# Kernel optimization log

Measured on AMD Instinct MI355X. Metric: run time of the kernel, lower is better.

## Reference

```python
import jax, jax.numpy as jnp
import numpy as np

NUM_HEADS = 8
KERNEL_SEARCH = 5  # local attention window
EPS = 1e-5


def _layernorm(x, g, b):
    m = jnp.mean(x, axis=-1, keepdims=True)
    v = jnp.var(x, axis=-1, keepdims=True)
    return (x - m) / jnp.sqrt(v + EPS) * g + b


def _unfold3(x):
    # x: [N, C, H, W] -> [N, C*9, H*W]; matches torch F.unfold(kernel=3, pad=1)
    # ordering: channel-major, kernel position (row-major) minor.
    N, C, H, W = x.shape
    xp = jnp.pad(x, ((0, 0), (0, 0), (1, 1), (1, 1)))
    pats = jnp.stack([xp[:, :, i:i + H, j:j + W] for i in range(3) for j in range(3)], axis=2)
    return pats.reshape(N, C * 9, H * W)


def _sai2token(x, w_mlp):
    # x: [b, c, a, h, w] -> tokens [h*w, b*a, spa_dim]
    b, c, a, h, w = x.shape
    x = x.transpose(0, 2, 1, 3, 4).reshape(b * a, c, h, w)
    tok = _unfold3(x).transpose(2, 0, 1)  # [hw, b*a, c*9]
    return jnp.einsum('lnk,ek->lne', tok, w_mlp)


def _local_mask(h, w, k):
    # additive mask [h*w, h*w]: 0 inside local kxk window, -inf outside
    kl, kr = k // 2, k - k // 2
    ii = jnp.arange(h)
    jj = jnp.arange(w)
    okh = (ii[None, :] >= ii[:, None] - kl) & (ii[None, :] < ii[:, None] + kr)  # [h,h]
    okw = (jj[None, :] >= jj[:, None] - kl) & (jj[None, :] < jj[:, None] + kr)  # [w,w]
    ok = okh[:, None, :, None] & okw[None, :, None, :]  # [h,w,h,w]
    ok = ok.reshape(h * w, h * w)
    return jnp.where(ok, 0.0, -jnp.inf).astype(jnp.float32)


def _attention(qk_in, v_in, in_proj_w, out_proj_w, bias):
    # qk_in/v_in: [L, B, E]; torch nn.MultiheadAttention, no biases, eval mode
    L, B, E = qk_in.shape
    Dh = E // NUM_HEADS
    Wq, Wk, Wv = in_proj_w[:E], in_proj_w[E:2 * E], in_proj_w[2 * E:]
    q = jnp.einsum('lbe,fe->lbf', qk_in, Wq).reshape(L, B, NUM_HEADS, Dh)
    k = jnp.einsum('lbe,fe->lbf', qk_in, Wk).reshape(L, B, NUM_HEADS, Dh)
    v = jnp.einsum('lbe,fe->lbf', v_in, Wv).reshape(L, B, NUM_HEADS, Dh)
    scale = 1.0 / np.sqrt(Dh).astype(np.float32)
    scores = jnp.einsum('lbhd,mbhd->bhlm', q, k) * scale + bias[None, None]
    attn = jax.nn.softmax(scores, axis=-1)
    out = jnp.einsum('bhlm,mbhd->lbhd', attn, v).reshape(L, B, E)
    return jnp.einsum('lbe,fe->lbf', out, out_proj_w)


def reference(buffer, spa_position, w_mlp, ln1_g, ln1_b, in_proj_w, out_proj_w,
              ln2_g, ln2_b, ff_w1, ff_w2, conv_w):
    b, c, a, h, w = buffer.shape
    bias = _local_mask(h, w, KERNEL_SEARCH)
    tok = _sai2token(buffer, w_mlp)          # [hw, b*a, E]
    pe = _sai2token(spa_position, w_mlp)
    x = _layernorm(tok + pe, ln1_g, ln1_b)
    tok = _attention(x, tok, in_proj_w, out_proj_w, bias) + tok
    # feed-forward (dropout is identity in eval)
    ff = _layernorm(tok, ln2_g, ln2_b)
    ff = jax.nn.relu(jnp.einsum('lbe,fe->lbf', ff, ff_w1))
    tok = jnp.einsum('lbf,ef->lbe', ff, ff_w2) + tok
    # Token2SAI: '(h w) (b a) e -> b e a h w' then 1x1x1 conv3d
    buf = tok.reshape(h, w, b, a, -1).transpose(2, 4, 3, 0, 1)  # [b, E, a, h, w]
    return jnp.einsum('oe,beahw->boahw', conv_w, buf)


def setup_inputs() -> dict:
    key = jax.random.key(0)
    ks = jax.random.split(key, 8)
    b, c, a, h, w = 1, 64, 25, 32, 32
    E = 2 * c
    s = 0.02
    return {
        'buffer': jax.random.normal(ks[0], (b, c, a, h, w), jnp.float32),
        'spa_position': jax.random.normal(ks[1], (b, c, a, h, w), jnp.float32),
        'w_mlp': jax.random.normal(ks[2], (E, c * 9), jnp.float32) * s,
        'ln1_g': jnp.ones((E,), jnp.float32),
        'ln1_b': jnp.zeros((E,), jnp.float32),
        'in_proj_w': jax.random.normal(ks[3], (3 * E, E), jnp.float32) * s,
        'out_proj_w': jax.random.normal(ks[4], (E, E), jnp.float32) * s,
        'ln2_g': jnp.ones((E,), jnp.float32),
        'ln2_b': jnp.zeros((E,), jnp.float32),
        'ff_w1': jax.random.normal(ks[5], (2 * E, E), jnp.float32) * s,
        'ff_w2': jax.random.normal(ks[6], (E, 2 * E), jnp.float32) * s,
        'conv_w': jax.random.normal(ks[7], (c, E), jnp.float32) * s,
    }
```

## Files before the change

kernel.cpp:

```cpp
#include <hip/hip_runtime.h>
#include <math.h>

#define Lh 32
#define Lw 32
#define LL 1024
#define BN 25
#define EE 128
#define CC 64
#define NHD 8
#define DH 16
#define FFD 256
#define MROWS 25600

typedef __attribute__((ext_vector_type(8))) short short8;
typedef __attribute__((ext_vector_type(4))) float f32x4;

__device__ inline ushort f2b(float x) {
    union { float f; unsigned u; } v; v.f = x;
    unsigned r = (v.u + 0x7fffu + ((v.u >> 16) & 1u)) >> 16;
    return (ushort)r;
}
__device__ inline float b2f(ushort u) {
    union { unsigned u; float f; } v; v.u = ((unsigned)u) << 16;
    return v.f;
}

#define OFF_W2  0
#define OFF_WQK 73728
#define OFF_WV  106496
#define OFF_WO  122880
#define OFF_W1  139264
#define OFF_W2F 172032
#define OFF_WC  204800
#define W_TOTAL 212992

__global__ __launch_bounds__(256) void k_prep(
    const float* __restrict__ w_mlp, const float* __restrict__ in_proj,
    const float* __restrict__ out_proj, const float* __restrict__ ff_w1,
    const float* __restrict__ ff_w2, const float* __restrict__ conv_w,
    ushort* __restrict__ Wb)
{
    int i = blockIdx.x * 256 + threadIdx.x;
    if (i >= W_TOTAL) return;
    if (i < 73728) {
        int e = i / 576, k = i - e * 576;
        int tap = k >> 6, ch = k & 63;
        Wb[OFF_W2 + i] = f2b(w_mlp[e * 576 + ch * 9 + tap]);
        return;
    }
    i -= 73728;
    if (i < 32768) {
        float v = in_proj[i];
        Wb[OFF_WQK + i] = f2b(i < 16384 ? v * 0.25f : v);
        return;
    }
    i -= 32768;
    if (i < 16384) { Wb[OFF_WV + i] = f2b(in_proj[32768 + i]); return; }
    i -= 16384;
    if (i < 16384) {
        int e = i >> 7, kpos = i & 127;
        int c = kpos >> 5, q = (kpos >> 3) & 3, ii = kpos & 7;
        int orig = (2 * c + (ii >> 2)) * 16 + q * 4 + (ii & 3);
        Wb[OFF_WO + i] = f2b(out_proj[e * 128 + orig]);
        return;
    }
    i -= 16384;
    if (i < 32768) { Wb[OFF_W1 + i] = f2b(ff_w1[i]); return; }
    i -= 32768;
    if (i < 32768) {
        int e = i >> 8, kpos = i & 255;
        int c = kpos >> 5, q = (kpos >> 3) & 3, ii = kpos & 7;
        int orig = (2 * c + (ii >> 2)) * 16 + q * 4 + (ii & 3);
        Wb[OFF_W2F + i] = f2b(ff_w2[e * 256 + orig]);
        return;
    }
    i -= 32768;
    {
        int o = i >> 7, kpos = i & 127;
        int c = kpos >> 5, q = (kpos >> 3) & 3, ii = kpos & 7;
        int orig = (2 * c + (ii >> 2)) * 16 + q * 4 + (ii & 3);
        Wb[OFF_WC + i] = f2b(conv_w[o * 128 + orig]);
    }
}

__global__ __launch_bounds__(256, 3) void k_tok_qkv(
    const float* __restrict__ buf, const float* __restrict__ spa,
    const ushort* __restrict__ W2, const ushort* __restrict__ WQK,
    const ushort* __restrict__ WV, const float* __restrict__ g1,
    const float* __restrict__ b1, ushort* __restrict__ TOKb,
    ushort* __restrict__ Qh, ushort* __restrict__ Kh, ushort* __restrict__ VTg)
{
    const int bid = blockIdx.x;
    const int idx = (bid & 7) * 100 + (bid >> 3);
    const int n = idx / 32, y = idx & 31;
    __shared__ ushort At[3 * 34 * 72];
    __shared__ ushort As_[3 * 34 * 72];
    __shared__ ushort Xs[32 * 136];
    __shared__ ushort Vs[32 * 136];
    __shared__ float2 red[32][4];
    float* t0 = (float*)Xs;
    float* t1 = (float*)Vs;
    const int t = threadIdx.x;
    const uint4 z = make_uint4(0, 0, 0, 0);

    for (int dy = 0; dy < 3; dy++) {
        int yy = y + dy - 1;
        if (yy >= 0 && yy < Lh) {
            {
                int ch = t >> 2, x8 = (t & 3) * 8;
                const float* p = buf + ((size_t)(ch * BN + n) * LL + yy * Lw + x8);
                const float* q = spa + ((size_t)(ch * BN + n) * LL + yy * Lw + x8);
                float4 a0 = ((const float4*)p)[0], a1 = ((const float4*)p)[1];
                float4 b0 = ((const float4*)q)[0], b1 = ((const float4*)q)[1];
                float* d0 = t0 + ch * 33 + x8;
                float* d1 = t1 + ch * 33 + x8;
                d0[0] = a0.x; d0[1] = a0.y; d0[2] = a0.z; d0[3] = a0.w;
                d0[4] = a1.x; d0[5] = a1.y; d0[6] = a1.z; d0[7] = a1.w;
                d1[0] = a0.x + b0.x; d1[1] = a0.y + b0.y; d1[2] = a0.z + b0.z; d1[3] = a0.w + b0.w;
                d1[4] = a1.x + b1.x; d1[5] = a1.y + b1.y; d1[6] = a1.z + b1.z; d1[7] = a1.w + b1.w;
            }
            __syncthreads();
            {
                int x = t >> 3, c8 = (t & 7) * 8;
                union { ushort u[8]; uint4 v; } o0, o1;
#pragma unroll
                for (int j = 0; j < 8; j++) {
                    o0.u[j] = f2b(t0[(c8 + j) * 33 + x]);
                    o1.u[j] = f2b(t1[(c8 + j) * 33 + x]);
                }
                *(uint4*)(At + (dy * 34 + x + 1) * 72 + c8) = o0.v;
                *(uint4*)(As_ + (dy * 34 + x + 1) * 72 + c8) = o1.v;
            }
            __syncthreads();
        } else {
            int x = t >> 3, c8 = (t & 7) * 8;
            *(uint4*)(At + (dy * 34 + x + 1) * 72 + c8) = z;
            *(uint4*)(As_ + (dy * 34 + x + 1) * 72 + c8) = z;
        }
    }
    if (t < 48) {
        int dy = t / 16, rem = t % 16;
        int colp = (rem >> 3) * 33, c8p = (rem & 7) * 8;
        *(uint4*)(At + (dy * 34 + colp) * 72 + c8p) = z;
        *(uint4*)(As_ + (dy * 34 + colp) * 72 + c8p) = z;
    }
    __syncthreads();

    const int w = t >> 6, lane = t & 63;
    const int col = lane & 15, quad = lane >> 4;
    f32x4 accT[2][2] = {}, accS[2][2] = {};

    for (int tap = 0; tap < 9; tap++) {
        int dy = tap / 3, dx = tap % 3;
#pragma unroll
        for (int cc = 0; cc < 2; cc++) {
            int kg = tap * 64 + cc * 32 + quad * 8;
            short8 b0 = *(const short8*)(W2 + (size_t)(w * 32 + col) * 576 + kg);
            short8 bq = *(const short8*)(W2 + (size_t)(w * 32 + 16 + col) * 576 + kg);
            int abase = (dy * 34 + col + dx) * 72 + cc * 32 + quad * 8;
            short8 aT0 = *(const short8*)(At + abase);
            short8 aT1 = *(const short8*)(At + abase + 16 * 72);
            short8 aS0 = *(const short8*)(As_ + abase);
            short8 aS1 = *(const short8*)(As_ + abase + 16 * 72);
            accT[0][0] = __builtin_amdgcn_mfma_f32_16x16x32_bf16(aT0, b0, accT[0][0], 0, 0, 0);
            accT[0][1] = __builtin_amdgcn_mfma_f32_16x16x32_bf16(aT0, bq, accT[0][1], 0, 0, 0);
            accT[1][0] = __builtin_amdgcn_mfma_f32_16x16x32_bf16(aT1, b0, accT[1][0], 0, 0, 0);
            accT[1][1] = __builtin_amdgcn_mfma_f32_16x16x32_bf16(aT1, bq, accT[1][1], 0, 0, 0);
            accS[0][0] = __builtin_amdgcn_mfma_f32_16x16x32_bf16(aS0, b0, accS[0][0], 0, 0, 0);
            accS[0][1] = __builtin_amdgcn_mfma_f32_16x16x32_bf16(aS0, bq, accS[0][1], 0, 0, 0);
            accS[1][0] = __builtin_amdgcn_mfma_f32_16x16x32_bf16(aS1, b0, accS[1][0], 0, 0, 0);
            accS[1][1] = __builtin_amdgcn_mfma_f32_16x16x32_bf16(aS1, bq, accS[1][1], 0, 0, 0);
        }
    }

#pragma unroll
    for (int mi = 0; mi < 2; mi++)
#pragma unroll
        for (int r = 0; r < 4; r++) {
            float a0 = accS[mi][0][r], a1 = accS[mi][1][r];
            float ss = a0 + a1, qq = a0 * a0 + a1 * a1;
#pragma unroll
            for (int m = 1; m < 16; m <<= 1) {
                ss += __shfl_xor(ss, m, 64);
                qq += __shfl_xor(qq, m, 64);
            }
            if (col == 0) red[mi * 16 + quad * 4 + r][w] = make_float2(ss, qq);
        }
    __syncthreads();

    const float ga = g1[w * 32 + col],      ba = b1[w * 32 + col];
    const float gb = g1[w * 32 + 16 + col], bb = b1[w * 32 + 16 + col];
#pragma unroll
    for (int mi = 0; mi < 2; mi++)
#pragma unroll
        for (int r = 0; r < 4; r++) {
            int x = mi * 16 + quad * 4 + r;
            float2 p0 = red[x][0], p1 = red[x][1], p2 = red[x][2], p3 = red[x][3];
            float mean = (p0.x + p1.x + p2.x + p3.x) * (1.f / 128.f);
            float var  = (p0.y + p1.y + p2.y + p3.y) * (1.f / 128.f) - mean * mean;
            float rstd = rsqrtf(var + 1e-5f);
            int e0 = w * 32 + col, e1 = w * 32 + 16 + col;
            Xs[x * 136 + e0] = f2b((accS[mi][0][r] - mean) * rstd * ga + ba);
            Xs[x * 136 + e1] = f2b((accS[mi][1][r] - mean) * rstd * gb + bb);
            Vs[x * 136 + e0] = f2b(accT[mi][0][r]);
            Vs[x * 136 + e1] = f2b(accT[mi][1][r]);
        }
    __syncthreads();

    short8 xb[2][4], xv[2][4];
#pragma unroll
    for (int j = 0; j < 2; j++)
#pragma unroll
        for (int kc = 0; kc < 4; kc++) {
            xb[j][kc] = *(const short8*)(Xs + (j * 16 + col) * 136 + kc * 32 + quad * 8);
            xv[j][kc] = *(const short8*)(Vs + (j * 16 + col) * 136 + kc * 32 + quad * 8);
        }
    f32x4 Q[2][2] = {}, K[2][2] = {}, V[2][2] = {};
#pragma unroll
    for (int hj = 0; hj < 2; hj++) {
        int h = 2 * w + hj;
#pragma unroll
        for (int kc = 0; kc < 4; kc++) {
            short8 aq = *(const short8*)(WQK + (size_t)(h * 16 + col) * 128 + kc * 32 + quad * 8);
            short8 ak = *(const short8*)(WQK + (size_t)(128 + h * 16 + col) * 128 + kc * 32 + quad * 8);
            short8 av = *(const short8*)(WV + (size_t)(h * 16 + col) * 128 + kc * 32 + quad * 8);
#pragma unroll
            for (int j = 0; j < 2; j++) {
                Q[hj][j] = __builtin_amdgcn_mfma_f32_16x16x32_bf16(aq, xb[j][kc], Q[hj][j], 0, 0, 0);
                K[hj][j] = __builtin_amdgcn_mfma_f32_16x16x32_bf16(ak, xb[j][kc], K[hj][j], 0, 0, 0);
                V[hj][j] = __builtin_amdgcn_mfma_f32_16x16x32_bf16(av, xv[j][kc], V[hj][j], 0, 0, 0);
            }
        }
    }
    ushort* VTs = At;
#pragma unroll
    for (int hj = 0; hj < 2; hj++) {
        int h = 2 * w + hj;
#pragma unroll
        for (int j = 0; j < 2; j++) {
            int l = y * 32 + j * 16 + col;
            size_t base = ((size_t)(n * 8 + h) * 1024 + l) * 16 + quad * 4;
            ushort4 oq, ok;
            oq.x = f2b(Q[hj][j][0]); oq.y = f2b(Q[hj][j][1]); oq.z = f2b(Q[hj][j][2]); oq.w = f2b(Q[hj][j][3]);
            ok.x = f2b(K[hj][j][0]); ok.y = f2b(K[hj][j][1]); ok.z = f2b(K[hj][j][2]); ok.w = f2b(K[hj][j][3]);
            *(ushort4*)(Qh + base) = oq;
            *(ushort4*)(Kh + base) = ok;
            int xp = ((col >> 2) << 3) + (j << 2) + (col & 3);
#pragma unroll
            for (int r = 0; r < 4; r++)
                VTs[(h * 16 + quad * 4 + r) * 34 + xp] = f2b(V[hj][j][r]);
        }
    }
#pragma unroll
    for (int k = 0; k < 2; k++) {
        int idx2 = t + k * 256;
        int r = idx2 >> 4, seg = idx2 & 15;
        *(uint4*)(TOKb + ((size_t)((y * 32 + r) * 25 + n)) * 128 + seg * 8) =
            *(const uint4*)(Vs + r * 136 + seg * 8);
    }
    __syncthreads();
    {
        int h = t >> 5, rem = t & 31, d = rem >> 1, xh = (rem & 1) * 16;
        size_t vrow = ((size_t)(n * 8 + h) * 32 + y) * 512;
        union { ushort u[8]; uint4 v; } o0, o1;
#pragma unroll
        for (int j = 0; j < 8; j++) {
            o0.u[j] = VTs[(h * 16 + d) * 34 + xh + j];
            o1.u[j] = VTs[(h * 16 + d) * 34 + xh + 8 + j];
        }
        *(uint4*)(VTg + vrow + d * 32 + xh)     = o0.v;
        *(uint4*)(VTg + vrow + d * 32 + xh + 8) = o1.v;
    }
}

__global__ __launch_bounds__(256, 4) void k_attn_ffn(
    const ushort* __restrict__ Qh, const ushort* __restrict__ Kh,
    const ushort* __restrict__ VTg, const ushort* __restrict__ WOP,
    const float* __restrict__ g2, const float* __restrict__ b2,
    const ushort* __restrict__ W1, const ushort* __restrict__ W2P,
    const ushort* __restrict__ WCP, const ushort* __restrict__ TOKb,
    float* __restrict__ out)
{
    __shared__ ushort OX[16 * 136];
    __shared__ ushort Rs[16 * 136];
    __shared__ ushort Hs[16 * 264];
    __shared__ float2 red[16][4];
    ushort* Ys = Rs;
    const int bid = blockIdx.x;
    const int idx = (bid & 7) * 200 + (bid >> 3);
    const int n = idx / 64, rem = idx & 63;
    const int y = rem >> 1, half = rem & 1;
    const int l0 = y * 32 + half * 16;
    const int t = threadIdx.x, w = t >> 6, lane = t & 63;
    const int col = lane & 15, quad = lane >> 4;
    const int qx = half * 16 + col;

    {
        int r = t >> 4, seg = t & 15;
        *(uint4*)(Rs + r * 136 + seg * 8) =
            *(const uint4*)(TOKb + ((size_t)((l0 + r) * 25 + n)) * 128 + seg * 8);
    }

    unsigned long long mbits = 0;
#pragma unroll
    for (int tt = 0; tt < 10; tt++) {
        int yy = y - 2 + (tt >> 1);
        bool rok = (yy >= 0) && (yy < 32);
        int kxb = ((tt & 1) << 4) + quad * 4;
#pragma unroll
        for (int r = 0; r < 4; r++) {
            int dd = kxb + r - qx;
            if (rok && ((unsigned)(dd + 2) <= 4u))
                mbits |= 1ull << (tt * 4 + r);
        }
    }

    short8 z8 = {0, 0, 0, 0, 0, 0, 0, 0};
    const size_t base0 = (size_t)(n * 8 + 2 * w) * 1024;
    const size_t base1 = base0 + 1024;
    const size_t vbase0 = (size_t)(n * 8 + 2 * w) * 32 * 512;
    const size_t vbase1 = vbase0 + 32 * 512;

    short8 qf0 = z8, qf1 = z8;
    if (quad < 2) {
        qf0 = *(const short8*)(Qh + (base0 + y * 32 + half * 16 + col) * 16 + quad * 8);
        qf1 = *(const short8*)(Qh + (base1 + y * 32 + half * 16 + col) * 16 + quad * 8);
    }

    union { ushort u[8]; short8 s; } pb0[5], pb1[5];
    float sum0 = 0.f, sum1 = 0.f;
#pragma unroll
    for (int kr = 0; kr < 5; kr++) {
        int yyc = min(max(y - 2 + kr, 0), 31);
        short8 kf0a = z8, kf0b = z8, kf1a = z8, kf1b = z8;
        if (quad < 2) {
            kf0a = *(const short8*)(Kh + (base0 + yyc * 32 + col) * 16 + quad * 8);
            kf0b = *(const short8*)(Kh + (base0 + yyc * 32 + 16 + col) * 16 + quad * 8);
            kf1a = *(const short8*)(Kh + (base1 + yyc * 32 + col) * 16 + quad * 8);
            kf1b = *(const short8*)(Kh + (base1 + yyc * 32 + 16 + col) * 16 + quad * 8);
        }
        f32x4 S00 = {}, S01 = {}, S10 = {}, S11 = {};
        S00 = __builtin_amdgcn_mfma_f32_16x16x32_bf16(kf0a, qf0, S00, 0, 0, 0);
        S01 = __builtin_amdgcn_mfma_f32_16x16x32_bf16(kf0b, qf0, S01, 0, 0, 0);
        S10 = __builtin_amdgcn_mfma_f32_16x16x32_bf16(kf1a, qf1, S10, 0, 0, 0);
        S11 = __builtin_amdgcn_mfma_f32_16x16x32_bf16(kf1b, qf1, S11, 0, 0, 0);
#pragma unroll
        for (int i = 0; i < 8; i++) {
            int tt = 2 * kr + (i >> 2), r = i & 3;
            bool ok = (mbits >> (tt * 4 + r)) & 1;
            float s0 = (i >= 4) ? S01[r] : S00[r];
            float s1 = (i >= 4) ? S11[r] : S10[r];
            float p0 = ok ? __expf(s0) : 0.f;
            float p1 = ok ? __expf(s1) : 0.f;
            pb0[kr].u[i] = f2b(p0);
            pb1[kr].u[i] = f2b(p1);
            sum0 += p0; sum1 += p1;
        }
    }
    sum0 += __shfl_xor(sum0, 16, 64); sum0 += __shfl_xor(sum0, 32, 64);
    sum1 += __shfl_xor(sum1, 16, 64); sum1 += __shfl_xor(sum1, 32, 64);
    const float inv0 = 1.f / sum0, inv1 = 1.f / sum1;

    f32x4 O20 = {}, O21 = {};
#pragma unroll
    for (int c = 0; c < 5; c++) {
        int yyc = min(max(y - 2 + c, 0), 31);
        short8 vt0 = *(const short8*)(VTg + vbase0 + (size_t)yyc * 512 + col * 32 + quad * 8);
        short8 vt1 = *(const short8*)(VTg + vbase1 + (size_t)yyc * 512 + col * 32 + quad * 8);
        O20 = __builtin_amdgcn_mfma_f32_16x16x32_bf16(vt0, pb0[c].s, O20, 0, 0, 0);
        O21 = __builtin_amdgcn_mfma_f32_16x16x32_bf16(vt1, pb1[c].s, O21, 0, 0, 0);
    }

    short8 wop[2][4];
#pragma unroll
    for (int jj = 0; jj < 2; jj++)
#pragma unroll
        for (int kc = 0; kc < 4; kc++)
            wop[jj][kc] = *(const short8*)(WOP + (size_t)((2 * w + jj) * 16 + col) * 128 + kc * 32 + quad * 8);

#pragma unroll
    for (int r = 0; r < 4; r++) { O20[r] *= inv0; O21[r] *= inv1; }

    {
        union { ushort u[8]; uint4 v; } pb;
#pragma unroll
        for (int i = 0; i < 4; i++) { pb.u[i] = f2b(O20[i]); pb.u[4 + i] = f2b(O21[i]); }
        *(uint4*)(OX + col * 136 + w * 32 + quad * 8) = pb.v;
    }
    __syncthreads();

    f32x4 Y[2] = {};
#pragma unroll
    for (int kc = 0; kc < 4; kc++) {
        short8 hb = *(const short8*)(OX + col * 136 + kc * 32 + quad * 8);
#pragma unroll
        for (int jj = 0; jj < 2; jj++)
            Y[jj] = __builtin_amdgcn_mfma_f32_16x16x32_bf16(wop[jj][kc], hb, Y[jj], 0, 0, 0);
    }

    short8 w1p[2][4];
#pragma unroll
    for (int j2 = 0; j2 < 2; j2++)
#pragma unroll
        for (int kc = 0; kc < 4; kc++)
            w1p[j2][kc] = *(const short8*)(W1 + (size_t)((4 * w + j2) * 16 + col) * 128 + kc * 32 + quad * 8);

    float sum = 0.f, sq = 0.f;
#pragma unroll
    for (int jj = 0; jj < 2; jj++)
#pragma unroll
        for (int r = 0; r < 4; r++) {
            int e = (2 * w + jj) * 16 + quad * 4 + r;
            float v = Y[jj][r] + b2f(Rs[col * 136 + e]);
            Y[jj][r] = v;
            sum += v; sq += v * v;
        }
    sum += __shfl_xor(sum, 16, 64); sum += __shfl_xor(sum, 32, 64);
    sq  += __shfl_xor(sq, 16, 64);  sq  += __shfl_xor(sq, 32, 64);
    if (quad == 0) red[col][w] = make_float2(sum, sq);
    __syncthreads();

    {
        float2 p0 = red[col][0], p1 = red[col][1], p2 = red[col][2], p3 = red[col][3];
        float mean = (p0.x + p1.x + p2.x + p3.x) * (1.f / 128.f);
        float var  = (p0.y + p1.y + p2.y + p3.y) * (1.f / 128.f) - mean * mean;
        float rstd = rsqrtf(var + 1e-5f);
#pragma unroll
        for (int jj = 0; jj < 2; jj++)
#pragma unroll
            for (int r = 0; r < 4; r++) {
                int e = (2 * w + jj) * 16 + quad * 4 + r;
                OX[col * 136 + e] = f2b((Y[jj][r] - mean) * rstd * g2[e] + b2[e]);
            }
    }
    __syncthreads();

    short8 xb[4];
#pragma unroll
    for (int kc = 0; kc < 4; kc++)
        xb[kc] = *(const short8*)(OX + col * 136 + kc * 32 + quad * 8);
    f32x4 H[4] = {};
#pragma unroll
    for (int j = 0; j < 4; j++) {
        int ft = 4 * w + j;
#pragma unroll
        for (int kc = 0; kc < 4; kc++) {
            short8 a = (j < 2) ? w1p[j][kc]
                     : *(const short8*)(W1 + (size_t)(ft * 16 + col) * 128 + kc * 32 + quad * 8);
            H[j] = __builtin_amdgcn_mfma_f32_16x16x32_bf16(a, xb[kc], H[j], 0, 0, 0);
        }
    }

    short8 w2pp[2][4];
#pragma unroll
    for (int j = 0; j < 2; j++)
#pragma unroll
        for (int kc = 0; kc < 4; kc++)
            w2pp[j][kc] = *(const short8*)(W2P + (size_t)((2 * w + j) * 16 + col) * 256 + kc * 32 + quad * 8);

#pragma unroll
    for (int cc = 0; cc < 2; cc++) {
        union { ushort u[8]; uint4 v; } pb;
#pragma unroll
        for (int i = 0; i < 8; i++)
            pb.u[i] = f2b(fmaxf(H[2 * cc + (i >> 2)][i & 3], 0.f));
        *(uint4*)(Hs + col * 264 + (2 * w + cc) * 32 + quad * 8) = pb.v;
    }
    __syncthreads();

    f32x4 Y2[2] = {};
#pragma unroll
    for (int kc = 0; kc < 8; kc++) {
        short8 hb = *(const short8*)(Hs + col * 264 + kc * 32 + quad * 8);
#pragma unroll
        for (int j = 0; j < 2; j++) {
            short8 a = (kc < 4) ? w2pp[j][kc]
                     : *(const short8*)(W2P + (size_t)((2 * w + j) * 16 + col) * 256 + kc * 32 + quad * 8);
            Y2[j] = __builtin_amdgcn_mfma_f32_16x16x32_bf16(a, hb, Y2[j], 0, 0, 0);
        }
    }

    short8 wcp[4];
#pragma unroll
    for (int c = 0; c < 4; c++)
        wcp[c] = *(const short8*)(WCP + (size_t)(w * 16 + col) * 128 + c * 32 + quad * 8);

    {
        union { ushort u[8]; uint4 v; } pb;
#pragma unroll
        for (int i = 0; i < 8; i++)
            pb.u[i] = f2b(Y2[i >> 2][i & 3] + Y[i >> 2][i & 3]);
        *(uint4*)(Ys + col * 136 + w * 32 + quad * 8) = pb.v;
    }
    __syncthreads();

    f32x4 O = {};
#pragma unroll
    for (int c = 0; c < 4; c++) {
        short8 yb = *(const short8*)(Ys + col * 136 + c * 32 + quad * 8);
        O = __builtin_amdgcn_mfma_f32_16x16x32_bf16(wcp[c], yb, O, 0, 0, 0);
    }
    const int l = l0 + col;
#pragma unroll
    for (int r2 = 0; r2 < 4; r2++) {
        int o = w * 16 + quad * 4 + r2;
        out[(size_t)(o * 25 + n) * 1024 + l] = O[r2];
    }
}

extern "C" void kernel_launch(void* const* d_in, const int* in_sizes, int n_in,
                              void* d_out, int out_size, void* d_ws, size_t ws_size,
                              hipStream_t stream)
{
    const float* buffer   = (const float*)d_in[0];
    const float* spa      = (const float*)d_in[1];
    const float* w_mlp    = (const float*)d_in[2];
    const float* ln1_g    = (const float*)d_in[3];
    const float* ln1_b    = (const float*)d_in[4];
    const float* in_proj  = (const float*)d_in[5];
    const float* out_proj = (const float*)d_in[6];
    const float* ln2_g    = (const float*)d_in[7];
    const float* ln2_b    = (const float*)d_in[8];
    const float* ff_w1    = (const float*)d_in[9];
    const float* ff_w2    = (const float*)d_in[10];
    const float* conv_w   = (const float*)d_in[11];
    float* out = (float*)d_out;

    char* ws = (char*)d_ws;
    ushort* TOKb = (ushort*)(ws);
    ushort* Qh   = (ushort*)(ws + 6553600);
    ushort* Kh   = (ushort*)(ws + 13107200);
    ushort* VTg  = (ushort*)(ws + 19660800);
    ushort* Wb   = (ushort*)(ws + 26214400);

    k_prep<<<dim3((W_TOTAL + 255) / 256), 256, 0, stream>>>(
        w_mlp, in_proj, out_proj, ff_w1, ff_w2, conv_w, Wb);
    k_tok_qkv<<<dim3(800), 256, 0, stream>>>(buffer, spa, Wb + OFF_W2,
                                             Wb + OFF_WQK, Wb + OFF_WV,
                                             ln1_g, ln1_b, TOKb, Qh, Kh, VTg);
    k_attn_ffn<<<dim3(1600), 256, 0, stream>>>(Qh, Kh, VTg, Wb + OFF_WO,
                                               ln2_g, ln2_b, Wb + OFF_W1,
                                               Wb + OFF_W2F, Wb + OFF_WC,
                                               TOKb, out);
}
```

Baseline: 169.6 us.

## Process 32 tokens per block in attention-FFN kernel to reuse weights

Each block of the fused attention/FFN kernel now handles a full image row of 32 tokens, two 16-token halves, instead of 16, and the grid is halved to 800 blocks. Weight fragments for the out-projection, FFN and conv are loaded once per block and applied to both halves. This cuts global weight traffic per token and improves MFMA issue density. In exchange it uses more registers and shared memory per block, which may lower occupancy, and there are fewer blocks to spread across CUs.

Result: faster. 160.5 us, median of 2 (-5.4%).

```diff
diff --git a/kernel.cpp b/kernel.cpp
--- a/kernel.cpp
+++ b/kernel.cpp
@@ -281,37 +281,24 @@
     const ushort* __restrict__ WCP, const ushort* __restrict__ TOKb,
     float* __restrict__ out)
 {
-    __shared__ ushort OX[16 * 136];
-    __shared__ ushort Rs[16 * 136];
-    __shared__ ushort Hs[16 * 264];
-    __shared__ float2 red[16][4];
+    __shared__ ushort OX[32 * 136];
+    __shared__ ushort Rs[32 * 136];
+    __shared__ ushort Hs[32 * 264];
+    __shared__ float2 red[32][4];
     ushort* Ys = Rs;
     const int bid = blockIdx.x;
-    const int idx = (bid & 7) * 200 + (bid >> 3);
-    const int n = idx / 64, rem = idx & 63;
-    const int y = rem >> 1, half = rem & 1;
-    const int l0 = y * 32 + half * 16;
+    const int idx = (bid & 7) * 100 + (bid >> 3);
+    const int n = idx / 32, y = idx & 31;
     const int t = threadIdx.x, w = t >> 6, lane = t & 63;
     const int col = lane & 15, quad = lane >> 4;
-    const int qx = half * 16 + col;
 
     {
-        int r = t >> 4, seg = t & 15;
-        *(uint4*)(Rs + r * 136 + seg * 8) =
-            *(const uint4*)(TOKb + ((size_t)((l0 + r) * 25 + n)) * 128 + seg * 8);
-    }
-
-    unsigned long long mbits = 0;
-#pragma unroll
-    for (int tt = 0; tt < 10; tt++) {
-        int yy = y - 2 + (tt >> 1);
-        bool rok = (yy >= 0) && (yy < 32);
-        int kxb = ((tt & 1) << 4) + quad * 4;
-#pragma unroll
-        for (int r = 0; r < 4; r++) {
-            int dd = kxb + r - qx;
-            if (rok && ((unsigned)(dd + 2) <= 4u))
-                mbits |= 1ull << (tt * 4 + r);
+#pragma unroll
+        for (int k = 0; k < 2; k++) {
+            int idx2 = t + k * 256;
+            int r = idx2 >> 4, seg = idx2 & 15;
+            *(uint4*)(Rs + r * 136 + seg * 8) =
+                *(const uint4*)(TOKb + ((size_t)((y * 32 + r) * 25 + n)) * 128 + seg * 8);
         }
     }
 
@@ -321,81 +308,102 @@
     const size_t vbase0 = (size_t)(n * 8 + 2 * w) * 32 * 512;
     const size_t vbase1 = vbase0 + 32 * 512;
 
-    short8 qf0 = z8, qf1 = z8;
-    if (quad < 2) {
-        qf0 = *(const short8*)(Qh + (base0 + y * 32 + half * 16 + col) * 16 + quad * 8);
-        qf1 = *(const short8*)(Qh + (base1 + y * 32 + half * 16 + col) * 16 + quad * 8);
-    }
-
-    union { ushort u[8]; short8 s; } pb0[5], pb1[5];
-    float sum0 = 0.f, sum1 = 0.f;
-#pragma unroll
-    for (int kr = 0; kr < 5; kr++) {
-        int yyc = min(max(y - 2 + kr, 0), 31);
-        short8 kf0a = z8, kf0b = z8, kf1a = z8, kf1b = z8;
+    short8 wop[2][4];
+
+#pragma unroll
+    for (int half = 0; half < 2; half++) {
+        const int qx = half * 16 + col;
+        unsigned long long mbits = 0;
+#pragma unroll
+        for (int tt = 0; tt < 10; tt++) {
+            int yy = y - 2 + (tt >> 1);
+            bool rok = (yy >= 0) && (yy < 32);
+            int kxb = ((tt & 1) << 4) + quad * 4;
+#pragma unroll
+            for (int r = 0; r < 4; r++) {
+                int dd = kxb + r - qx;
+                if (rok && ((unsigned)(dd + 2) <= 4u))
+                    mbits |= 1ull << (tt * 4 + r);
+            }
+        }
+
+        short8 qf0 = z8, qf1 = z8;
         if (quad < 2) {
-            kf0a = *(const short8*)(Kh + (base0 + yyc * 32 + col) * 16 + quad * 8);
-            kf0b = *(const short8*)(Kh + (base0 + yyc * 32 + 16 + col) * 16 + quad * 8);
-            kf1a = *(const short8*)(Kh + (base1 + yyc * 32 + col) * 16 + quad * 8);
-            kf1b = *(const short8*)(Kh + (base1 + yyc * 32 + 16 + col) * 16 + quad * 8);
-        }
-        f32x4 S00 = {}, S01 = {}, S10 = {}, S11 = {};
-        S00 = __builtin_amdgcn_mfma_f32_16x16x32_bf16(kf0a, qf0, S00, 0, 0, 0);
-        S01 = __builtin_amdgcn_mfma_f32_16x16x32_bf16(kf0b, qf0, S01, 0, 0, 0);
-        S10 = __builtin_amdgcn_mfma_f32_16x16x32_bf16(kf1a, qf1, S10, 0, 0, 0);
-        S11 = __builtin_amdgcn_mfma_f32_16x16x32_bf16(kf1b, qf1, S11, 0, 0, 0);
-#pragma unroll
-        for (int i = 0; i < 8; i++) {
-            int tt = 2 * kr + (i >> 2), r = i & 3;
-            bool ok = (mbits >> (tt * 4 + r)) & 1;
-            float s0 = (i >= 4) ? S01[r] : S00[r];
-            float s1 = (i >= 4) ? S11[r] : S10[r];
-            float p0 = ok ? __expf(s0) : 0.f;
-            float p1 = ok ? __expf(s1) : 0.f;
-            pb0[kr].u[i] = f2b(p0);
-            pb1[kr].u[i] = f2b(p1);
-            sum0 += p0; sum1 += p1;
-        }
-    }
-    sum0 += __shfl_xor(sum0, 16, 64); sum0 += __shfl_xor(sum0, 32, 64);
-    sum1 += __shfl_xor(sum1, 16, 64); sum1 += __shfl_xor(sum1, 32, 64);
-    const float inv0 = 1.f / sum0, inv1 = 1.f / sum1;
-
-    f32x4 O20 = {}, O21 = {};
-#pragma unroll
-    for (int c = 0; c < 5; c++) {
-        int yyc = min(max(y - 2 + c, 0), 31);
-        short8 vt0 = *(const short8*)(VTg + vbase0 + (size_t)yyc * 512 + col * 32 + quad * 8);
-        short8 vt1 = *(const short8*)(VTg + vbase1 + (size_t)yyc * 512 + col * 32 + quad * 8);
-        O20 = __builtin_amdgcn_mfma_f32_16x16x32_bf16(vt0, pb0[c].s, O20, 0, 0, 0);
-        O21 = __builtin_amdgcn_mfma_f32_16x16x32_bf16(vt1, pb1[c].s, O21, 0, 0, 0);
-    }
-
-    short8 wop[2][4];
-#pragma unroll
-    for (int jj = 0; jj < 2; jj++)
-#pragma unroll
-        for (int kc = 0; kc < 4; kc++)
-            wop[jj][kc] = *(const short8*)(WOP + (size_t)((2 * w + jj) * 16 + col) * 128 + kc * 32 + quad * 8);
-
-#pragma unroll
-    for (int r = 0; r < 4; r++) { O20[r] *= inv0; O21[r] *= inv1; }
-
-    {
-        union { ushort u[8]; uint4 v; } pb;
-#pragma unroll
-        for (int i = 0; i < 4; i++) { pb.u[i] = f2b(O20[i]); pb.u[4 + i] = f2b(O21[i]); }
-        *(uint4*)(OX + col * 136 + w * 32 + quad * 8) = pb.v;
-    }
-    __syncthreads();
-
-    f32x4 Y[2] = {};
+            qf0 = *(const short8*)(Qh + (base0 + y * 32 + half * 16 + col) * 16 + quad * 8);
+            qf1 = *(const short8*)(Qh + (base1 + y * 32 + half * 16 + col) * 16 + quad * 8);
+        }
+
+        union { ushort u[8]; short8 s; } pb0[5], pb1[5];
+        float sum0 = 0.f, sum1 = 0.f;
+#pragma unroll
+        for (int kr = 0; kr < 5; kr++) {
+            int yyc = min(max(y - 2 + kr, 0), 31);
+            short8 kf0a = z8, kf0b = z8, kf1a = z8, kf1b = z8;
+            if (quad < 2) {
+                kf0a = *(const short8*)(Kh + (base0 + yyc * 32 + col) * 16 + quad * 8);
+                kf0b = *(const short8*)(Kh + (base0 + yyc * 32 + 16 + col) * 16 + quad * 8);
+                kf1a = *(const short8*)(Kh + (base1 + yyc * 32 + col) * 16 + quad * 8);
+                kf1b = *(const short8*)(Kh + (base1 + yyc * 32 + 16 + col) * 16 + quad * 8);
+            }
+            f32x4 S00 = {}, S01 = {}, S10 = {}, S11 = {};
+            S00 = __builtin_amdgcn_mfma_f32_16x16x32_bf16(kf0a, qf0, S00, 0, 0, 0);
+            S01 = __builtin_amdgcn_mfma_f32_16x16x32_bf16(kf0b, qf0, S01, 0, 0, 0);
+            S10 = __builtin_amdgcn_mfma_f32_16x16x32_bf16(kf1a, qf1, S10, 0, 0, 0);
+            S11 = __builtin_amdgcn_mfma_f32_16x16x32_bf16(kf1b, qf1, S11, 0, 0, 0);
+#pragma unroll
+            for (int i = 0; i < 8; i++) {
+                int tt = 2 * kr + (i >> 2), r = i & 3;
+                bool ok = (mbits >> (tt * 4 + r)) & 1;
+                float s0 = (i >= 4) ? S01[r] : S00[r];
+                float s1 = (i >= 4) ? S11[r] : S10[r];
+                float p0 = ok ? __expf(s0) : 0.f;
+                float p1 = ok ? __expf(s1) : 0.f;
+                pb0[kr].u[i] = f2b(p0);
+                pb1[kr].u[i] = f2b(p1);
+                sum0 += p0; sum1 += p1;
+            }
+        }
+        sum0 += __shfl_xor(sum0, 16, 64); sum0 += __shfl_xor(sum0, 32, 64);
+        sum1 += __shfl_xor(sum1, 16, 64); sum1 += __shfl_xor(sum1, 32, 64);
+        const float inv0 = 1.f / sum0, inv1 = 1.f / sum1;
+
+        if (half == 1) {
+#pragma unroll
+            for (int jj = 0; jj < 2; jj++)
+#pragma unroll
+                for (int kc = 0; kc < 4; kc++)
+                    wop[jj][kc] = *(const short8*)(WOP + (size_t)((2 * w + jj) * 16 + col) * 128 + kc * 32 + quad * 8);
+        }
+
+        f32x4 O20 = {}, O21 = {};
+#pragma unroll
+        for (int c = 0; c < 5; c++) {
+            int yyc = min(max(y - 2 + c, 0), 31);
+            short8 vt0 = *(const short8*)(VTg + vbase0 + (size_t)yyc * 512 + col * 32 + quad * 8);
+            short8 vt1 = *(const short8*)(VTg + vbase1 + (size_t)yyc * 512 + col * 32 + quad * 8);
+            O20 = __builtin_amdgcn_mfma_f32_16x16x32_bf16(vt0, pb0[c].s, O20, 0, 0, 0);
+            O21 = __builtin_amdgcn_mfma_f32_16x16x32_bf16(vt1, pb1[c].s, O21, 0, 0, 0);
+        }
+#pragma unroll
+        for (int r = 0; r < 4; r++) { O20[r] *= inv0; O21[r] *= inv1; }
+
+        union { ushort u[8]; uint4 v; } pk;
+#pragma unroll
+        for (int i = 0; i < 4; i++) { pk.u[i] = f2b(O20[i]); pk.u[4 + i] = f2b(O21[i]); }
+        *(uint4*)(OX + (half * 16 + col) * 136 + w * 32 + quad * 8) = pk.v;
+    }
+    __syncthreads();
+
+    f32x4 Y[2][2] = {};
 #pragma unroll
     for (int kc = 0; kc < 4; kc++) {
-        short8 hb = *(const short8*)(OX + col * 136 + kc * 32 + quad * 8);
-#pragma unroll
-        for (int jj = 0; jj < 2; jj++)
-            Y[jj] = __builtin_amdgcn_mfma_f32_16x16x32_bf16(wop[jj][kc], hb, Y[jj], 0, 0, 0);
+        short8 hb0 = *(const short8*)(OX + col * 136 + kc * 32 + quad * 8);
+        short8 hb1 = *(const short8*)(OX + (16 + col) * 136 + kc * 32 + quad * 8);
+#pragma unroll
+        for (int jj = 0; jj < 2; jj++) {
+            Y[jj][0] = __builtin_amdgcn_mfma_f32_16x16x32_bf16(wop[jj][kc], hb0, Y[jj][0], 0, 0, 0);
+            Y[jj][1] = __builtin_amdgcn_mfma_f32_16x16x32_bf16(wop[jj][kc], hb1, Y[jj][1], 0, 0, 0);
+        }
     }
 
     short8 w1p[2][4];
@@ -405,23 +413,28 @@
         for (int kc = 0; kc < 4; kc++)
             w1p[j2][kc] = *(const short8*)(W1 + (size_t)((4 * w + j2) * 16 + col) * 128 + kc * 32 + quad * 8);
 
-    float sum = 0.f, sq = 0.f;
-#pragma unroll
-    for (int jj = 0; jj < 2; jj++)
-#pragma unroll
-        for (int r = 0; r < 4; r++) {
-            int e = (2 * w + jj) * 16 + quad * 4 + r;
-            float v = Y[jj][r] + b2f(Rs[col * 136 + e]);
-            Y[jj][r] = v;
-            sum += v; sq += v * v;
-        }
-    sum += __shfl_xor(sum, 16, 64); sum += __shfl_xor(sum, 32, 64);
-    sq  += __shfl_xor(sq, 16, 64);  sq  += __shfl_xor(sq, 32, 64);
-    if (quad == 0) red[col][w] = make_float2(sum, sq);
-    __syncthreads();
-
-    {
-        float2 p0 = red[col][0], p1 = red[col][1], p2 = red[col][2], p3 = red[col][3];
+#pragma unroll
+    for (int tt = 0; tt < 2; tt++) {
+        float sum = 0.f, sq = 0.f;
+#pragma unroll
+        for (int jj = 0; jj < 2; jj++)
+#pragma unroll
+            for (int r = 0; r < 4; r++) {
+                int e = (2 * w + jj) * 16 + quad * 4 + r;
+                float v = Y[jj][tt][r] + b2f(Rs[(tt * 16 + col) * 136 + e]);
+                Y[jj][tt][r] = v;
+                sum += v; sq += v * v;
+            }
+        sum += __shfl_xor(sum, 16, 64); sum += __shfl_xor(sum, 32, 64);
+        sq  += __shfl_xor(sq, 16, 64);  sq  += __shfl_xor(sq, 32, 64);
+        if (quad == 0) red[tt * 16 + col][w] = make_float2(sum, sq);
+    }
+    __syncthreads();
+
+#pragma unroll
+    for (int tt = 0; tt < 2; tt++) {
+        int tok = tt * 16 + col;
+        float2 p0 = red[tok][0], p1 = red[tok][1], p2 = red[tok][2], p3 = red[tok][3];
         float mean = (p0.x + p1.x + p2.x + p3.x) * (1.f / 128.f);
         float var  = (p0.y + p1.y + p2.y + p3.y) * (1.f / 128.f) - mean * mean;
         float rstd = rsqrtf(var + 1e-5f);
@@ -430,24 +443,34 @@
 #pragma unroll
             for (int r = 0; r < 4; r++) {
                 int e = (2 * w + jj) * 16 + quad * 4 + r;
-                OX[col * 136 + e] = f2b((Y[jj][r] - mean) * rstd * g2[e] + b2[e]);
-            }
-    }
-    __syncthreads();
-
-    short8 xb[4];
-#pragma unroll
-    for (int kc = 0; kc < 4; kc++)
-        xb[kc] = *(const short8*)(OX + col * 136 + kc * 32 + quad * 8);
-    f32x4 H[4] = {};
-#pragma unroll
-    for (int j = 0; j < 4; j++) {
-        int ft = 4 * w + j;
-#pragma unroll
-        for (int kc = 0; kc < 4; kc++) {
-            short8 a = (j < 2) ? w1p[j][kc]
-                     : *(const short8*)(W1 + (size_t)(ft * 16 + col) * 128 + kc * 32 + quad * 8);
-            H[j] = __builtin_amdgcn_mfma_f32_16x16x32_bf16(a, xb[kc], H[j], 0, 0, 0);
+                OX[tok * 136 + e] = f2b((Y[jj][tt][r] - mean) * rstd * g2[e] + b2[e]);
+            }
+    }
+    __syncthreads();
+
+#pragma unroll
+    for (int tt = 0; tt < 2; tt++) {
+        short8 xb[4];
+#pragma unroll
+        for (int kc = 0; kc < 4; kc++)
+            xb[kc] = *(const short8*)(OX + (tt * 16 + col) * 136 + kc * 32 + quad * 8);
+        f32x4 H[4] = {};
+#pragma unroll
+        for (int j = 0; j < 4; j++) {
+#pragma unroll
+            for (int kc = 0; kc < 4; kc++) {
+                short8 a = (j < 2) ? w1p[j][kc]
+                         : *(const short8*)(W1 + (size_t)((4 * w + j) * 16 + col) * 128 + kc * 32 + quad * 8);
+                H[j] = __builtin_amdgcn_mfma_f32_16x16x32_bf16(a, xb[kc], H[j], 0, 0, 0);
+            }
+        }
+#pragma unroll
+        for (int cc = 0; cc < 2; cc++) {
+            union { ushort u[8]; uint4 v; } pk;
+#pragma unroll
+            for (int i = 0; i < 8; i++)
+                pk.u[i] = f2b(fmaxf(H[2 * cc + (i >> 2)][i & 3], 0.f));
+            *(uint4*)(Hs + (tt * 16 + col) * 264 + (2 * w + cc) * 32 + quad * 8) = pk.v;
         }
     }
 
@@ -457,26 +480,19 @@
 #pragma unroll
         for (int kc = 0; kc < 4; kc++)
             w2pp[j][kc] = *(const short8*)(W2P + (size_t)((2 * w + j) * 16 + col) * 256 + kc * 32 + quad * 8);
-
-#pragma unroll
-    for (int cc = 0; cc < 2; cc++) {
-        union { ushort u[8]; uint4 v; } pb;
-#pragma unroll
-        for (int i = 0; i < 8; i++)
-            pb.u[i] = f2b(fmaxf(H[2 * cc + (i >> 2)][i & 3], 0.f));
-        *(uint4*)(Hs + col * 264 + (2 * w + cc) * 32 + quad * 8) = pb.v;
-    }
-    __syncthreads();
-
-    f32x4 Y2[2] = {};
+    __syncthreads();
+
+    f32x4 Y2[2][2] = {};
 #pragma unroll
     for (int kc = 0; kc < 8; kc++) {
-        short8 hb = *(const short8*)(Hs + col * 264 + kc * 32 + quad * 8);
+        short8 hb0 = *(const short8*)(Hs + col * 264 + kc * 32 + quad * 8);
+        short8 hb1 = *(const short8*)(Hs + (16 + col) * 264 + kc * 32 + quad * 8);
 #pragma unroll
         for (int j = 0; j < 2; j++) {
             short8 a = (kc < 4) ? w2pp[j][kc]
                      : *(const short8*)(W2P + (size_t)((2 * w + j) * 16 + col) * 256 + kc * 32 + quad * 8);
-            Y2[j] = __builtin_amdgcn_mfma_f32_16x16x32_bf16(a, hb, Y2[j], 0, 0, 0);
+            Y2[j][0] = __builtin_amdgcn_mfma_f32_16x16x32_bf16(a, hb0, Y2[j][0], 0, 0, 0);
+            Y2[j][1] = __builtin_amdgcn_mfma_f32_16x16x32_bf16(a, hb1, Y2[j][1], 0, 0, 0);
         }
     }
 
@@ -485,26 +501,32 @@
     for (int c = 0; c < 4; c++)
         wcp[c] = *(const short8*)(WCP + (size_t)(w * 16 + col) * 128 + c * 32 + quad * 8);
 
-    {
-        union { ushort u[8]; uint4 v; } pb;
+#pragma unroll
+    for (int tt = 0; tt < 2; tt++) {
+        union { ushort u[8]; uint4 v; } pk;
 #pragma unroll
         for (int i = 0; i < 8; i++)
-            pb.u[i] = f2b(Y2[i >> 2][i & 3] + Y[i >> 2][i & 3]);
-        *(uint4*)(Ys + col * 136 + w * 32 + quad * 8) = pb.v;
-    }
-    __syncthreads();
-
-    f32x4 O = {};
+            pk.u[i] = f2b(Y2[i >> 2][tt][i & 3] + Y[i >> 2][tt][i & 3]);
+        *(uint4*)(Ys + (tt * 16 + col) * 136 + w * 32 + quad * 8) = pk.v;
+    }
+    __syncthreads();
+
+    f32x4 O[2] = {};
 #pragma unroll
     for (int c = 0; c < 4; c++) {
-        short8 yb = *(const short8*)(Ys + col * 136 + c * 32 + quad * 8);
-        O = __builtin_amdgcn_mfma_f32_16x16x32_bf16(wcp[c], yb, O, 0, 0, 0);
-    }
-    const int l = l0 + col;
-#pragma unroll
-    for (int r2 = 0; r2 < 4; r2++) {
-        int o = w * 16 + quad * 4 + r2;
-        out[(size_t)(o * 25 + n) * 1024 + l] = O[r2];
+        short8 yb0 = *(const short8*)(Ys + col * 136 + c * 32 + quad * 8);
+        short8 yb1 = *(const short8*)(Ys + (16 + col) * 136 + c * 32 + quad * 8);
+        O[0] = __builtin_amdgcn_mfma_f32_16x16x32_bf16(wcp[c], yb0, O[0], 0, 0, 0);
+        O[1] = __builtin_amdgcn_mfma_f32_16x16x32_bf16(wcp[c], yb1, O[1], 0, 0, 0);
+    }
+#pragma unroll
+    for (int tt = 0; tt < 2; tt++) {
+        int l = y * 32 + tt * 16 + col;
+#pragma unroll
+        for (int r2 = 0; r2 < 4; r2++) {
+            int o = w * 16 + quad * 4 + r2;
+            out[(size_t)(o * 25 + n) * 1024 + l] = O[tt][r2];
+        }
     }
 }
 
@@ -538,8 +560,8 @@
     k_tok_qkv<<<dim3(800), 256, 0, stream>>>(buffer, spa, Wb + OFF_W2,
                                              Wb + OFF_WQK, Wb + OFF_WV,
                                              ln1_g, ln1_b, TOKb, Qh, Kh, VTg);
-    k_attn_ffn<<<dim3(1600), 256, 0, stream>>>(Qh, Kh, VTg, Wb + OFF_WO,
-                                               ln2_g, ln2_b, Wb + OFF_W1,
-                                               Wb + OFF_W2F, Wb + OFF_WC,
-                                               TOKb, out);
+    k_attn_ffn<<<dim3(800), 256, 0, stream>>>(Qh, Kh, VTg, Wb + OFF_WO,
+                                              ln2_g, ln2_b, Wb + OFF_W1,
+                                              Wb + OFF_W2F, Wb + OFF_WC,
+                                              TOKb, out);
 }
```
